# Performance work log

Hardware: AMD Instinct MI355X
Metric: run time of the kernel (lower is better)

The kernel has to match this reference:

```python
import jax, jax.numpy as jnp
import numpy as np

B, N, C = 2, 384, 11            # images, proposals/img, classes (incl background)
RCN = 5                          # (xc, yc, w, h, angle_deg)
WEIGHTS = (10.0, 10.0, 5.0, 5.0, 1.0)
SCORE_THRESH = 0.05
NMS_THRESH = 0.5
DET_PER_IMG = 100
BBOX_XFORM_CLIP = float(np.log(1000.0 / 16.0))
EPS = 1e-8


def setup_inputs() -> dict:
    key = jax.random.key(0)
    k1, k2, k3, k4, k5 = jax.random.split(key, 5)
    class_logits = jax.random.normal(k1, (B * N, C), jnp.float32) * 2.0
    box_regression = jax.random.normal(k2, (B * N, C * RCN), jnp.float32) * 0.5
    xy = jax.random.uniform(k3, (B * N, 2), jnp.float32, 0.0, 1024.0)
    wh = jax.random.uniform(k4, (B * N, 2), jnp.float32, 16.0, 256.0)
    ang = jax.random.uniform(k5, (B * N, 1), jnp.float32, -90.0, 90.0)
    rrects = jnp.concatenate([xy, wh, ang], -1)
    return {"class_logits": class_logits, "box_regression": box_regression, "rrects": rrects}


def cross2(a, b):
    return a[..., 0] * b[..., 1] - a[..., 1] * b[..., 0]


def decode(rel, anchors):
    # rel (...,5) deltas, anchors (...,5) rotated boxes; relative angle coder
    wx, wy, ww, wh, wa = WEIGHTS
    dx = rel[..., 0] / wx
    dy = rel[..., 1] / wy
    dw = jnp.clip(rel[..., 2] / ww, None, BBOX_XFORM_CLIP)
    dh = jnp.clip(rel[..., 3] / wh, None, BBOX_XFORM_CLIP)
    da = rel[..., 4] / wa
    xc, yc, w, h, a = (anchors[..., i] for i in range(5))
    px = dx * w + xc
    py = dy * h + yc
    pw = jnp.exp(dw) * w
    ph = jnp.exp(dh) * h
    pa = da * (180.0 / np.pi) + a
    pa = (pa + 180.0) % 360.0 - 180.0
    return jnp.stack([px, py, pw, ph, pa], -1)


def corners(b):
    # (...,5) -> (...,4,2) rectangle corners (CCW in box frame)
    xc, yc, w, h, a = (b[..., i] for i in range(5))
    t = a * (np.pi / 180.0)
    c, s = jnp.cos(t), jnp.sin(t)
    hx, hy = w * 0.5, h * 0.5
    lx = jnp.stack([-hx, hx, hx, -hx], -1)
    ly = jnp.stack([-hy, -hy, hy, hy], -1)
    px = xc[..., None] + lx * c[..., None] - ly * s[..., None]
    py = yc[..., None] + lx * s[..., None] + ly * c[..., None]
    return jnp.stack([px, py], -1)


def inter_area(ca, cb):
    # intersection area of two convex quads (4,2),(4,2): candidate points =
    # 16 edge-edge intersections + 8 contained corners, sorted by angle, shoelace
    a0, b0 = ca, cb
    d1 = jnp.roll(ca, -1, 0) - ca
    d2 = jnp.roll(cb, -1, 0) - cb
    den = cross2(d1[:, None, :], d2[None, :, :])                # (4,4)
    diff = b0[None, :, :] - a0[:, None, :]
    den_s = jnp.where(jnp.abs(den) < EPS, 1.0, den)
    t = cross2(diff, d2[None, :, :]) / den_s
    u = cross2(diff, d1[:, None, :]) / den_s
    ok = (jnp.abs(den) >= EPS) & (t >= 0) & (t <= 1) & (u >= 0) & (u <= 1)
    pint = a0[:, None, :] + t[..., None] * d1[:, None, :]       # (4,4,2)

    def inside(p, cs):
        ev = jnp.roll(cs, -1, 0) - cs
        cr = cross2(ev[None, :, :], p[:, None, :] - cs[None, :, :])  # (4,4)
        return jnp.all(cr >= -1e-6, -1) | jnp.all(cr <= 1e-6, -1)

    pts = jnp.concatenate([pint.reshape(16, 2), ca, cb], 0)     # (24,2)
    msk = jnp.concatenate([ok.reshape(16), inside(ca, cb), inside(cb, ca)], 0)
    nv = jnp.sum(msk)
    cen = jnp.sum(pts * msk[:, None], 0) / jnp.maximum(nv, 1)
    pts = jnp.where(msk[:, None], pts, cen)                     # park invalid at centroid
    ang = jnp.arctan2(pts[:, 1] - cen[1], pts[:, 0] - cen[0])
    p = pts[jnp.argsort(ang)]
    area = 0.5 * jnp.abs(jnp.sum(cross2(p, jnp.roll(p, -1, 0))))
    return jnp.where(nv >= 3, area, 0.0)


def rotated_iou_matrix(boxes):
    # boxes (N,5) -> (N,N) rotated IoU
    cs = corners(boxes)
    area = boxes[:, 2] * boxes[:, 3]
    inter = jax.vmap(lambda ci: jax.vmap(lambda cj: inter_area(ci, cj))(cs))(cs)
    return inter / (area[:, None] + area[None, :] - inter + EPS)


def greedy_nms(iou, scores, valid):
    n = iou.shape[0]
    order = jnp.argsort(-jnp.where(valid, scores, -jnp.inf))
    ios = iou[order][:, order]
    vs = valid[order]
    idx = jnp.arange(n)

    def body(i, sup):
        cur_ok = (~sup[i]) & vs[i]
        return sup | (cur_ok & (ios[i] > NMS_THRESH) & (idx > i))

    sup = jax.lax.fori_loop(0, n, body, jnp.zeros((n,), bool))
    keep_sorted = (~sup) & vs
    return jnp.zeros((n,), bool).at[order].set(keep_sorted)


def reference(class_logits, box_regression, rrects):
    prob = jax.nn.softmax(class_logits, -1)                     # (M,C)
    rel = box_regression.reshape(B * N, C, RCN)
    dec = decode(rel, rrects[:, None, :])                       # (M,C,5)
    boxes = dec.reshape(B, N, C, RCN)
    scores = prob.reshape(B, N, C)
    fg_boxes = jnp.moveaxis(boxes[:, :, 1:, :], 2, 1)           # (B,C-1,N,5)
    fg_scores = jnp.moveaxis(scores[:, :, 1:], 2, 1)            # (B,C-1,N)
    valid = fg_scores > SCORE_THRESH
    iou = jax.vmap(jax.vmap(rotated_iou_matrix))(fg_boxes)      # (B,C-1,N,N)
    keep = jax.vmap(jax.vmap(greedy_nms))(iou, fg_scores, valid)
    flat_scores = jnp.where(keep, fg_scores, -1.0).reshape(B, (C - 1) * N)
    top_s, top_i = jax.lax.top_k(flat_scores, DET_PER_IMG)
    sel_boxes = jnp.take_along_axis(fg_boxes.reshape(B, (C - 1) * N, RCN), top_i[:, :, None], axis=1)
    labels = top_i // N + 1
    ok = top_s > 0.0
    out = jnp.concatenate([jnp.where(ok[..., None], sel_boxes, 0.0), jnp.where(ok, top_s, 0.0)[..., None]], -1)
    labels = jnp.where(ok, labels, 0)
    return out, labels
```

## Files before the change

kernel.cpp:

```cpp
#include <hip/hip_runtime.h>
#include <cmath>

#define NPROP 384
#define NB 2
#define NCLS 11
#define NFG 10
#define BC_TOTAL (NB*NFG)
#define FLAT_PER_IMG (NFG*NPROP)
#define DET 100
#define PAIR_LDS_CAP 4096

#define OFF_BOXES 0
#define OFF_KIDX  38400
#define OFF_KSC   46080
#define OFF_KCNT  53760

typedef unsigned long long ull;

__device__ __forceinline__ void mk_corners(float px, float py, float pw, float ph, float pa,
                                           float cxo[4], float cyo[4]) {
    float t = pa * 0.017453292519943295f;
    float ct = cosf(t), st = sinf(t);
    float hx = pw*0.5f, hy = ph*0.5f;
    float lx[4] = {-hx, hx, hx, -hx};
    float ly[4] = {-hy, -hy, hy, hy};
#pragma unroll
    for (int k = 0; k < 4; ++k) {
        cxo[k] = px + lx[k]*ct - ly[k]*st;
        cyo[k] = py + lx[k]*st + ly[k]*ct;
    }
}

__device__ float inter_area_net(const float ax[4], const float ay[4],
                                const float bx[4], const float by[4]) {
    float d1x[4], d1y[4], d2x[4], d2y[4];
#pragma unroll
    for (int k = 0; k < 4; ++k) {
        int k1 = (k + 1) & 3;
        d1x[k] = ax[k1] - ax[k]; d1y[k] = ay[k1] - ay[k];
        d2x[k] = bx[k1] - bx[k]; d2y[k] = by[k1] - by[k];
    }
    float ex[32], ey[32];
    bool msk[24];
#pragma unroll
    for (int i = 0; i < 4; ++i) {
#pragma unroll
        for (int j = 0; j < 4; ++j) {
            float den = d1x[i]*d2y[j] - d1y[i]*d2x[j];
            float dfx = bx[j]-ax[i], dfy = by[j]-ay[i];
            float dens = (fabsf(den) < 1e-8f) ? 1.0f : den;
            float t = (dfx*d2y[j] - dfy*d2x[j]) / dens;
            float u = (dfx*d1y[i] - dfy*d1x[i]) / dens;
            bool ok = (fabsf(den) >= 1e-8f) && t >= 0.0f && t <= 1.0f
                                            && u >= 0.0f && u <= 1.0f;
            ex[i*4+j] = ax[i] + t*d1x[i];
            ey[i*4+j] = ay[i] + t*d1y[i];
            msk[i*4+j] = ok;
        }
    }
#pragma unroll
    for (int i = 0; i < 4; ++i) {
        bool allp = true, alln = true;
#pragma unroll
        for (int j = 0; j < 4; ++j) {
            float cr = d2x[j]*(ay[i]-by[j]) - d2y[j]*(ax[i]-bx[j]);
            allp = allp && (cr >= -1e-6f);
            alln = alln && (cr <= 1e-6f);
        }
        ex[16+i] = ax[i]; ey[16+i] = ay[i]; msk[16+i] = allp || alln;
    }
#pragma unroll
    for (int i = 0; i < 4; ++i) {
        bool allp = true, alln = true;
#pragma unroll
        for (int j = 0; j < 4; ++j) {
            float cr = d1x[j]*(by[i]-ay[j]) - d1y[j]*(bx[i]-ax[j]);
            allp = allp && (cr >= -1e-6f);
            alln = alln && (cr <= 1e-6f);
        }
        ex[20+i] = bx[i]; ey[20+i] = by[i]; msk[20+i] = allp || alln;
    }
    int nv = 0; float sx = 0.f, sy = 0.f;
#pragma unroll
    for (int k = 0; k < 24; ++k)
        if (msk[k]) { nv++; sx += ex[k]; sy += ey[k]; }
    float fm = (float)(nv > 1 ? nv : 1);
    float cx = sx / fm, cy = sy / fm;
    unsigned key[32];
#pragma unroll
    for (int k = 0; k < 24; ++k) {
        float qx = msk[k] ? ex[k] : cx;
        float qy = msk[k] ? ey[k] : cy;
        ex[k] = qx; ey[k] = qy;
        float dx = qx - cx, dy = qy - cy;
        float den = fabsf(dx) + fabsf(dy);
        float r = (den > 0.0f) ? dy / den : 0.0f;
        float p = (dx >= 0.0f) ? r : ((dy >= 0.0f) ? 2.0f - r : -2.0f - r);
        p = p + 0.0f;
        unsigned u = __float_as_uint(p);
        u = (u & 0x80000000u) ? ~u : (u | 0x80000000u);
        key[k] = (u & 0xFFFFFFE0u) | (unsigned)k;
    }
#pragma unroll
    for (int k = 24; k < 32; ++k) { key[k] = 0xFFFFFFFFu; ex[k] = 0.f; ey[k] = 0.f; }
#pragma unroll
    for (int k = 2; k <= 32; k <<= 1) {
#pragma unroll
        for (int j = k >> 1; j > 0; j >>= 1) {
#pragma unroll
            for (int i = 0; i < 32; ++i) {
                int l = i ^ j;
                if (l > i) {
                    bool up = ((i & k) == 0);
                    unsigned ka = key[i], kb = key[l];
                    bool sw = up ? (ka > kb) : (ka < kb);
                    float xa = ex[i], xb = ex[l];
                    float ya = ey[i], yb = ey[l];
                    key[i] = sw ? kb : ka; key[l] = sw ? ka : kb;
                    ex[i]  = sw ? xb : xa; ex[l]  = sw ? xa : xb;
                    ey[i]  = sw ? yb : ya; ey[l]  = sw ? ya : yb;
                }
            }
        }
    }
    float s = 0.f;
#pragma unroll
    for (int k = 0; k < 24; ++k) {
        int n = (k + 1 == 24) ? 0 : (k + 1);
        s += ex[k]*ey[n] - ey[k]*ex[n];
    }
    float area = 0.5f * fabsf(s);
    return (nv >= 3) ? area : 0.0f;
}

__device__ __forceinline__ void eval_pair_lds(const float* pxL, const float* pyL,
                                              const float* pwL, const float* phL,
                                              const float* paL, const float* areaL,
                                              ull* supL, int hi, int lo) {
    float axp[4], ayp[4], bxp[4], byp[4];
    mk_corners(pxL[hi], pyL[hi], pwL[hi], phL[hi], paL[hi], axp, ayp);
    mk_corners(pxL[lo], pyL[lo], pwL[lo], phL[lo], paL[lo], bxp, byp);
    float inter = inter_area_net(axp, ayp, bxp, byp);
    float iou = inter / (areaL[hi] + areaL[lo] - inter + 1e-8f);
    if (iou > 0.5f)
        atomicOr((unsigned int*)supL + hi*12 + (lo >> 5), 1u << (lo & 31));
}

__global__ __launch_bounds__(768)
void bc_kernel(const float* __restrict__ logits,
               const float* __restrict__ boxreg,
               const float* __restrict__ rrects,
               float* __restrict__ ws,
               float* __restrict__ out) {
    __shared__ float pxL[NPROP], pyL[NPROP], pwL[NPROP], phL[NPROP], paL[NPROP];
    __shared__ float areaL[NPROP], scoreL[NPROP];
    __shared__ float axhL[NPROP], ayhL[NPROP];
    __shared__ int   origL[NPROP];
    __shared__ unsigned pairL[PAIR_LDS_CAP];
    __shared__ ull   supL[NPROP*6];
    __shared__ ull   keyL[NPROP];
    __shared__ int   orderL[NPROP];
    __shared__ unsigned char keepS[NPROP];
    __shared__ int   wbase[16];
    __shared__ int   totS, pcntS;

    int bc = blockIdx.x, t = threadIdx.x;
    int b = bc / NFG, cls = (bc % NFG) + 1;
    int wv = t >> 6, lane = t & 63;

    int g = bc*768 + t;
    if (g < NB*DET*6 + NB*DET) out[g] = 0.0f;
    if (t == 0) { pcntS = 0; }
    for (int k = t; k < NPROP*6; k += 768) supL[k] = 0ull;

    float prob = 0.0f;
    if (t < NPROP) {
        int m = b*NPROP + t;
        float lg[NCLS];
        float mx = -INFINITY;
#pragma unroll
        for (int c = 0; c < NCLS; ++c) { lg[c] = logits[m*NCLS+c]; mx = fmaxf(mx, lg[c]); }
        float sum = 0.f;
#pragma unroll
        for (int c = 0; c < NCLS; ++c) sum += expf(lg[c]-mx);
        prob = expf(lg[cls]-mx) / sum;
        float axc = rrects[m*5+0], ayc = rrects[m*5+1];
        float aw  = rrects[m*5+2], ah  = rrects[m*5+3], aa = rrects[m*5+4];
        const float* rel = boxreg + m*(NCLS*5) + cls*5;
        float dx = rel[0] / 10.0f;
        float dy = rel[1] / 10.0f;
        float dw = fminf(rel[2] / 5.0f, 4.1351665567423205f);
        float dh = fminf(rel[3] / 5.0f, 4.1351665567423205f);
        float da = rel[4];
        float px = dx*aw + axc;
        float py = dy*ah + ayc;
        float pw = expf(dw)*aw;
        float ph = expf(dh)*ah;
        float pa = da*57.29577951308232f + aa;
        float xm = pa + 180.0f;
        float r = fmodf(xm, 360.0f);
        if (r < 0.0f) r += 360.0f;
        pa = r - 180.0f;
        pxL[t]=px; pyL[t]=py; pwL[t]=pw; phL[t]=ph; paL[t]=pa;
        areaL[t]=pw*ph; scoreL[t]=prob;
        float th = pa * 0.017453292519943295f;
        float ct = fabsf(cosf(th)), st = fabsf(sinf(th));
        axhL[t] = 0.5f*(pw*ct + ph*st);
        ayhL[t] = 0.5f*(pw*st + ph*ct);
        float* boxes = ws + OFF_BOXES;
        int o = bc*NPROP + t;
        boxes[o*5+0]=px; boxes[o*5+1]=py; boxes[o*5+2]=pw; boxes[o*5+3]=ph; boxes[o*5+4]=pa;
        bool vi = prob > 0.05f;
        keyL[t] = vi ? (((ull)__float_as_uint(prob) << 32) | (ull)(0xFFFFFFFFu - (unsigned)t))
                     : (ull)(0xFFFFFFFFu - (unsigned)t);
        keepS[t] = 0;
    }
    bool vi = (t < NPROP) && (prob > 0.05f);
    ull vb = __ballot(vi);
    if (lane == 0) wbase[wv] = __popcll(vb);
    __syncthreads();
    if (t == 0) {
        int s = 0;
#pragma unroll
        for (int w = 0; w < 6; ++w) { int c = wbase[w]; wbase[w] = s; s += c; }
        totS = s;
    }
    __syncthreads();
    if (vi) origL[wbase[wv] + (int)__popcll(vb & ((1ull << lane) - 1ull))] = t;
    __syncthreads();
    int cnt = totS;

    for (int a = wv; a < cnt; a += 12) {
        int ia = origL[a];
        float cxa = pxL[ia], cya = pyL[ia], Aa = areaL[ia], sa = scoreL[ia];
        float axa = axhL[ia], aya = ayhL[ia];
        for (int b0 = a + 1; b0 < cnt; b0 += 64) {
            int bb = b0 + lane;
            bool go = false; int ib = 0;
            if (bb < cnt) {
                ib = origL[bb];
                float ox = (axa + axhL[ib]) - fabsf(cxa - pxL[ib]);
                float oy = (aya + ayhL[ib]) - fabsf(cya - pyL[ib]);
                go = (ox > 0.0f) && (oy > 0.0f);
                if (go) {
                    float Ab = areaL[ib];
                    float ub = fminf(ox*oy, fminf(Aa, Ab));
                    go = (3.0f*ub > Aa + Ab);
                }
            }
            ull m = __ballot(go);
            int base = 0;
            if (lane == 0 && m) base = atomicAdd(&pcntS, __popcll(m));
            base = __shfl(base, 0);
            if (go) {
                float sb = scoreL[ib];
                bool afirst = (sa > sb) || (sa == sb && ia < ib);
                int hi = afirst ? ia : ib;
                int lo = afirst ? ib : ia;
                int pos = base + (int)__popcll(m & ((1ull << lane) - 1ull));
                if (pos < PAIR_LDS_CAP)
                    pairL[pos] = ((unsigned)hi << 16) | (unsigned)lo;
                else
                    eval_pair_lds(pxL, pyL, pwL, phL, paL, areaL, supL, hi, lo);
            }
        }
    }
    __syncthreads();

    {
        int np = pcntS; if (np > PAIR_LDS_CAP) np = PAIR_LDS_CAP;
        for (int p = t; p < np; p += 768) {
            unsigned pk = pairL[p];
            eval_pair_lds(pxL, pyL, pwL, phL, paL, areaL, supL,
                          (int)(pk >> 16), (int)(pk & 0xFFFFu));
        }
    }
    __syncthreads();

    if (t < NPROP) {
        ull myk = keyL[t];
        int r = 0;
        for (int k = 0; k < NPROP; k += 8) {
            int acc = 0;
#pragma unroll
            for (int q = 0; q < 8; ++q) acc += (keyL[k+q] > myk) ? 1 : 0;
            r += acc;
        }
        orderL[r] = t;
    }
    __syncthreads();

    if (t < 64) {
        int NV = cnt;
        int ord0 = orderL[lane],      ord1 = orderL[64+lane];
        int ord2 = orderL[128+lane],  ord3 = orderL[192+lane];
        int ord4 = orderL[256+lane],  ord5 = orderL[320+lane];
        ull mask = 0ull;
        int o_cur = __shfl(ord0, 0);
        ull row_cur = (lane < 6) ? supL[o_cur*6 + lane] : 0ull;
        for (int p = 0; p < NV; ++p) {
            int pn = (p + 1 < NPROP) ? (p + 1) : 0;
            int seg = pn >> 6, sl = pn & 63;
            int on = __shfl(ord0, sl);
            on = (seg == 1) ? __shfl(ord1, sl) : on;
            on = (seg == 2) ? __shfl(ord2, sl) : on;
            on = (seg == 3) ? __shfl(ord3, sl) : on;
            on = (seg == 4) ? __shfl(ord4, sl) : on;
            on = (seg == 5) ? __shfl(ord5, sl) : on;
            ull row_next = (lane < 6) ? supL[on*6 + lane] : 0ull;
            bool myhit = (lane == (o_cur >> 6)) && ((mask >> (o_cur & 63)) & 1ull);
            ull bal = __ballot(myhit);
            if (bal == 0ull) {
                if (lane == 0) keepS[o_cur] = 1;
                mask |= row_cur;
            }
            row_cur = row_next;
            o_cur = on;
        }
    }
    __syncthreads();

    bool kp = (t < NPROP) && (keepS[t] != 0);
    ull bal = __ballot(kp);
    if (lane == 0) wbase[wv] = __popcll(bal);
    __syncthreads();
    if (t == 0) {
        int s = 0;
#pragma unroll
        for (int w = 0; w < 6; ++w) { int c = wbase[w]; wbase[w] = s; s += c; }
        ((unsigned int*)(ws + OFF_KCNT))[bc] = (unsigned)s;
    }
    __syncthreads();
    if (kp) {
        int pos = wbase[wv] + (int)__popcll(bal & ((1ull << lane) - 1ull));
        ((unsigned int*)(ws + OFF_KIDX))[bc*NPROP + pos] = (unsigned)((bc % NFG)*NPROP + t);
        (ws + OFF_KSC)[bc*NPROP + pos] = scoreL[t];
    }
}

__global__ __launch_bounds__(256)
void topk_kernel(const float* __restrict__ ws, float* __restrict__ out) {
    __shared__ ull keyL[FLAT_PER_IMG];
    int b = blockIdx.x >> 4;
    int slice = blockIdx.x & 15;
    int t = threadIdx.x;
    const unsigned int* kidx2 = (const unsigned int*)(ws + OFF_KIDX);
    const float* ksc2 = ws + OFF_KSC;
    const unsigned int* kcnt2 = (const unsigned int*)(ws + OFF_KCNT);
    const float* boxes = ws + OFF_BOXES;
    int offs[NFG], cnts[NFG];
    int K = 0;
#pragma unroll
    for (int fg = 0; fg < NFG; ++fg) {
        cnts[fg] = (int)kcnt2[b*NFG + fg];
        offs[fg] = K;
        K += cnts[fg];
    }
#pragma unroll
    for (int fg = 0; fg < NFG; ++fg) {
        int bc = b*NFG + fg;
        for (int k = t; k < cnts[fg]; k += 256) {
            unsigned sb = __float_as_uint(ksc2[bc*NPROP + k]);
            unsigned f  = kidx2[bc*NPROP + k];
            keyL[offs[fg] + k] = ((ull)sb << 32) | (ull)(0xFFFFFFFFu - f);
        }
    }
    int KP = (K + 15) & ~15;
    for (int k = K + t; k < KP; k += 256) keyL[k] = 0ull;
    __syncthreads();
    int e = slice*256 + t;
    if (e >= K) return;
    ull my = keyL[e];
    int r = 0;
    for (int k = 0; k < KP; k += 16) {
        int acc = 0;
#pragma unroll
        for (int q = 0; q < 16; ++q)
            acc += (keyL[k+q] > my) ? 1 : 0;
        r += acc;
    }
    if (r < DET) {
        unsigned f = 0xFFFFFFFFu - (unsigned)(my & 0xFFFFFFFFu);
        float s = __uint_as_float((unsigned)(my >> 32));
        int src = b*FLAT_PER_IMG + (int)f;
        float* row = out + (b*DET + r)*6;
#pragma unroll
        for (int q = 0; q < 5; ++q) row[q] = boxes[src*5+q];
        row[5] = s;
        out[NB*DET*6 + b*DET + r] = (float)(f / NPROP + 1);
    }
}

extern "C" void kernel_launch(void* const* d_in, const int* in_sizes, int n_in,
                              void* d_out, int out_size, void* d_ws, size_t ws_size,
                              hipStream_t stream) {
    const float* logits = (const float*)d_in[0];
    const float* boxreg = (const float*)d_in[1];
    const float* rrects = (const float*)d_in[2];
    float* out = (float*)d_out;
    float* ws  = (float*)d_ws;
    (void)in_sizes; (void)n_in; (void)out_size; (void)ws_size;

    bc_kernel<<<BC_TOTAL, 768, 0, stream>>>(logits, boxreg, rrects, ws, out);
    topk_kernel<<<NB * 16, 256, 0, stream>>>(ws, out);
}
```

Baseline: 141.1 us.

## Split pairwise IoU work across eight blocks per class and add separate NMS kernel

Each (image, class) job now gets eight blocks. Each block decodes all boxes again and evaluates a strided subset of candidate pairs. Suppressing pairs go out to global workspace lists, and a new NMS kernel rebuilds the suppression bitmask from those lists before running the greedy scan. This spreads the heavy rotated-IoU work from 20 blocks over 160 so more compute units are busy. The cost is redundant decoding, an extra kernel launch, and a round trip through global memory for pairs that are capped per slice.

```diff
diff --git a/kernel.cpp b/kernel.cpp
--- a/kernel.cpp
+++ b/kernel.cpp
@@ -9,11 +9,16 @@
 #define FLAT_PER_IMG (NFG*NPROP)
 #define DET 100
 #define PAIR_LDS_CAP 4096
+#define NSLICE 8
+#define SLICE_CAP 9600
 
 #define OFF_BOXES 0
-#define OFF_KIDX  38400
-#define OFF_KSC   46080
-#define OFF_KCNT  53760
+#define OFF_SCORE 38400
+#define OFF_KIDX  46080
+#define OFF_KSC   53760
+#define OFF_KCNT  61440
+#define OFF_SCNT  61472
+#define OFF_SPAIR 61632
 
 typedef unsigned long long ull;
 
@@ -133,45 +138,30 @@
     return (nv >= 3) ? area : 0.0f;
 }
 
-__device__ __forceinline__ void eval_pair_lds(const float* pxL, const float* pyL,
-                                              const float* pwL, const float* phL,
-                                              const float* paL, const float* areaL,
-                                              ull* supL, int hi, int lo) {
-    float axp[4], ayp[4], bxp[4], byp[4];
-    mk_corners(pxL[hi], pyL[hi], pwL[hi], phL[hi], paL[hi], axp, ayp);
-    mk_corners(pxL[lo], pyL[lo], pwL[lo], phL[lo], paL[lo], bxp, byp);
-    float inter = inter_area_net(axp, ayp, bxp, byp);
-    float iou = inter / (areaL[hi] + areaL[lo] - inter + 1e-8f);
-    if (iou > 0.5f)
-        atomicOr((unsigned int*)supL + hi*12 + (lo >> 5), 1u << (lo & 31));
-}
-
 __global__ __launch_bounds__(768)
-void bc_kernel(const float* __restrict__ logits,
-               const float* __restrict__ boxreg,
-               const float* __restrict__ rrects,
-               float* __restrict__ ws,
-               float* __restrict__ out) {
+void pairheavy_kernel(const float* __restrict__ logits,
+                      const float* __restrict__ boxreg,
+                      const float* __restrict__ rrects,
+                      float* __restrict__ ws,
+                      float* __restrict__ out) {
     __shared__ float pxL[NPROP], pyL[NPROP], pwL[NPROP], phL[NPROP], paL[NPROP];
     __shared__ float areaL[NPROP], scoreL[NPROP];
     __shared__ float axhL[NPROP], ayhL[NPROP];
     __shared__ int   origL[NPROP];
     __shared__ unsigned pairL[PAIR_LDS_CAP];
-    __shared__ ull   supL[NPROP*6];
-    __shared__ ull   keyL[NPROP];
-    __shared__ int   orderL[NPROP];
-    __shared__ unsigned char keepS[NPROP];
     __shared__ int   wbase[16];
-    __shared__ int   totS, pcntS;
-
-    int bc = blockIdx.x, t = threadIdx.x;
+    __shared__ int   totS, pcntS, scntS;
+
+    int blk = blockIdx.x, t = threadIdx.x;
+    int bc = blk >> 3, slice = blk & 7;
     int b = bc / NFG, cls = (bc % NFG) + 1;
     int wv = t >> 6, lane = t & 63;
 
-    int g = bc*768 + t;
-    if (g < NB*DET*6 + NB*DET) out[g] = 0.0f;
-    if (t == 0) { pcntS = 0; }
-    for (int k = t; k < NPROP*6; k += 768) supL[k] = 0ull;
+    if (slice == 0) {
+        int g = bc*768 + t;
+        if (g < NB*DET*6 + NB*DET) out[g] = 0.0f;
+    }
+    if (t == 0) { pcntS = 0; scntS = 0; }
 
     float prob = 0.0f;
     if (t < NPROP) {
@@ -207,13 +197,12 @@
         float ct = fabsf(cosf(th)), st = fabsf(sinf(th));
         axhL[t] = 0.5f*(pw*ct + ph*st);
         ayhL[t] = 0.5f*(pw*st + ph*ct);
-        float* boxes = ws + OFF_BOXES;
-        int o = bc*NPROP + t;
-        boxes[o*5+0]=px; boxes[o*5+1]=py; boxes[o*5+2]=pw; boxes[o*5+3]=ph; boxes[o*5+4]=pa;
-        bool vi = prob > 0.05f;
-        keyL[t] = vi ? (((ull)__float_as_uint(prob) << 32) | (ull)(0xFFFFFFFFu - (unsigned)t))
-                     : (ull)(0xFFFFFFFFu - (unsigned)t);
-        keepS[t] = 0;
+        if (slice == 0) {
+            float* boxes = ws + OFF_BOXES;
+            int o = bc*NPROP + t;
+            boxes[o*5+0]=px; boxes[o*5+1]=py; boxes[o*5+2]=pw; boxes[o*5+3]=ph; boxes[o*5+4]=pa;
+            ws[OFF_SCORE + o] = prob;
+        }
     }
     bool vi = (t < NPROP) && (prob > 0.05f);
     ull vb = __ballot(vi);
@@ -230,7 +219,9 @@
     __syncthreads();
     int cnt = totS;
 
-    for (int a = wv; a < cnt; a += 12) {
+    unsigned int* spair = (unsigned int*)(ws + OFF_SPAIR) + (bc*NSLICE + slice)*SLICE_CAP;
+
+    for (int a = slice + 8*wv; a < cnt; a += 96) {
         int ia = origL[a];
         float cxa = pxL[ia], cya = pyL[ia], Aa = areaL[ia], sa = scoreL[ia];
         float axa = axhL[ia], aya = ayhL[ia];
@@ -258,10 +249,19 @@
                 int hi = afirst ? ia : ib;
                 int lo = afirst ? ib : ia;
                 int pos = base + (int)__popcll(m & ((1ull << lane) - 1ull));
-                if (pos < PAIR_LDS_CAP)
+                if (pos < PAIR_LDS_CAP) {
                     pairL[pos] = ((unsigned)hi << 16) | (unsigned)lo;
-                else
-                    eval_pair_lds(pxL, pyL, pwL, phL, paL, areaL, supL, hi, lo);
+                } else {
+                    float axp[4], ayp[4], bxp[4], byp[4];
+                    mk_corners(pxL[hi], pyL[hi], pwL[hi], phL[hi], paL[hi], axp, ayp);
+                    mk_corners(pxL[lo], pyL[lo], pwL[lo], phL[lo], paL[lo], bxp, byp);
+                    float inter = inter_area_net(axp, ayp, bxp, byp);
+                    float iou = inter / (areaL[hi] + areaL[lo] - inter + 1e-8f);
+                    if (iou > 0.5f) {
+                        int sp = atomicAdd(&scntS, 1);
+                        if (sp < SLICE_CAP) spair[sp] = ((unsigned)hi << 10) | (unsigned)lo;
+                    }
+                }
             }
         }
     }
@@ -271,14 +271,46 @@
         int np = pcntS; if (np > PAIR_LDS_CAP) np = PAIR_LDS_CAP;
         for (int p = t; p < np; p += 768) {
             unsigned pk = pairL[p];
-            eval_pair_lds(pxL, pyL, pwL, phL, paL, areaL, supL,
-                          (int)(pk >> 16), (int)(pk & 0xFFFFu));
-        }
-    }
-    __syncthreads();
-
-    if (t < NPROP) {
-        ull myk = keyL[t];
+            int hi = (int)(pk >> 16), lo = (int)(pk & 0xFFFFu);
+            float axp[4], ayp[4], bxp[4], byp[4];
+            mk_corners(pxL[hi], pyL[hi], pwL[hi], phL[hi], paL[hi], axp, ayp);
+            mk_corners(pxL[lo], pyL[lo], pwL[lo], phL[lo], paL[lo], bxp, byp);
+            float inter = inter_area_net(axp, ayp, bxp, byp);
+            float iou = inter / (areaL[hi] + areaL[lo] - inter + 1e-8f);
+            if (iou > 0.5f) {
+                int sp = atomicAdd(&scntS, 1);
+                if (sp < SLICE_CAP) spair[sp] = ((unsigned)hi << 10) | (unsigned)lo;
+            }
+        }
+    }
+    __syncthreads();
+    if (t == 0) {
+        int n = scntS; if (n > SLICE_CAP) n = SLICE_CAP;
+        ((unsigned int*)(ws + OFF_SCNT))[bc*NSLICE + slice] = (unsigned)n;
+    }
+}
+
+__global__ __launch_bounds__(384)
+void nms_kernel(float* __restrict__ ws) {
+    __shared__ ull keyL[NPROP];
+    __shared__ ull supL[NPROP*6];
+    __shared__ int orderL[NPROP];
+    __shared__ unsigned char keepS[NPROP];
+    __shared__ int wbase[8];
+    int bc = blockIdx.x, t = threadIdx.x;
+    int wv = t >> 6, lane = t & 63;
+    float sc = ws[OFF_SCORE + bc*NPROP + t];
+    bool vi = sc > 0.05f;
+    ull myk = vi ? (((ull)__float_as_uint(sc) << 32) | (ull)(0xFFFFFFFFu - (unsigned)t))
+                 : (ull)(0xFFFFFFFFu - (unsigned)t);
+    keyL[t] = myk;
+    keepS[t] = 0;
+    for (int k = t; k < NPROP*6; k += NPROP) supL[k] = 0ull;
+    ull vb = __ballot(vi);
+    if (lane == 0) wbase[wv] = __popcll(vb);
+    __syncthreads();
+    int NV = wbase[0] + wbase[1] + wbase[2] + wbase[3] + wbase[4] + wbase[5];
+    {
         int r = 0;
         for (int k = 0; k < NPROP; k += 8) {
             int acc = 0;
@@ -288,10 +320,20 @@
         }
         orderL[r] = t;
     }
-    __syncthreads();
-
+    const unsigned int* scnt = (const unsigned int*)(ws + OFF_SCNT);
+#pragma unroll
+    for (int s = 0; s < NSLICE; ++s) {
+        int n = (int)scnt[bc*NSLICE + s];
+        const unsigned int* spair = (const unsigned int*)(ws + OFF_SPAIR)
+                                    + (bc*NSLICE + s)*SLICE_CAP;
+        for (int k = t; k < n; k += NPROP) {
+            unsigned pk = spair[k];
+            int hi = (int)(pk >> 10), lo = (int)(pk & 0x3FFu);
+            atomicOr((unsigned int*)supL + hi*12 + (lo >> 5), 1u << (lo & 31));
+        }
+    }
+    __syncthreads();
     if (t < 64) {
-        int NV = cnt;
         int ord0 = orderL[lane],      ord1 = orderL[64+lane];
         int ord2 = orderL[128+lane],  ord3 = orderL[192+lane];
         int ord4 = orderL[256+lane],  ord5 = orderL[320+lane];
@@ -319,8 +361,7 @@
         }
     }
     __syncthreads();
-
-    bool kp = (t < NPROP) && (keepS[t] != 0);
+    bool kp = keepS[t] != 0;
     ull bal = __ballot(kp);
     if (lane == 0) wbase[wv] = __popcll(bal);
     __syncthreads();
@@ -334,7 +375,7 @@
     if (kp) {
         int pos = wbase[wv] + (int)__popcll(bal & ((1ull << lane) - 1ull));
         ((unsigned int*)(ws + OFF_KIDX))[bc*NPROP + pos] = (unsigned)((bc % NFG)*NPROP + t);
-        (ws + OFF_KSC)[bc*NPROP + pos] = scoreL[t];
+        (ws + OFF_KSC)[bc*NPROP + pos] = sc;
     }
 }
 
@@ -401,6 +442,7 @@
     float* ws  = (float*)d_ws;
     (void)in_sizes; (void)n_in; (void)out_size; (void)ws_size;
 
-    bc_kernel<<<BC_TOTAL, 768, 0, stream>>>(logits, boxreg, rrects, ws, out);
+    pairheavy_kernel<<<BC_TOTAL * NSLICE, 768, 0, stream>>>(logits, boxreg, rrects, ws, out);
+    nms_kernel<<<BC_TOTAL, NPROP, 0, stream>>>(ws);
     topk_kernel<<<NB * 16, 256, 0, stream>>>(ws, out);
 }
```

New measurement: 122.7 us, median of 2. -13.0%, faster.
